# Optimization experiments

Hardware: AMD Instinct MI355X
Metric: run time of the kernel (lower is better)

## Reference

```python
import jax, jax.numpy as jnp
import numpy as np

N_EXPERTS = 8
IN_DIM = 2048
HID_DIM = 4096  # max(IN_DIM*2, IN_DIM)
OUT_DIM = 2048
N_NODES = 16384


def setup_inputs() -> dict:
    key = jax.random.key(0)
    k1, k2, k3 = jax.random.split(key, 3)
    x = jax.random.normal(k1, (N_NODES, IN_DIM), dtype=jnp.float32)
    # nn.init.normal_(std=0.02); torch Linear stores weight as [out, in]
    W1 = jax.random.normal(k2, (N_EXPERTS, HID_DIM, IN_DIM), dtype=jnp.float32) * 0.02
    W2 = jax.random.normal(k3, (N_EXPERTS, OUT_DIM, HID_DIM), dtype=jnp.float32) * 0.02
    return {"expert_idx": 2, "x": x, "W1": W1, "W2": W2}


def reference(expert_idx, x, W1, W2):
    # Select this expert's weights (static index, matches ModuleList lookup)
    w1 = W1[expert_idx]  # [hid, in]
    w2 = W2[expert_idx]  # [out, hid]
    h = jnp.einsum('ni,hi->nh', x, w1)          # Linear(in->hid), bias=False
    h = jax.nn.gelu(h, approximate=False)        # torch nn.GELU default = exact erf
    out = jnp.einsum('nh,oh->no', h, w2)         # Linear(hid->out), bias=False
    return out
```

## Files before the change

### kernel.cpp

```cpp
#include <hip/hip_runtime.h>
#include <hip/hip_bf16.h>
#include <math.h>


typedef __bf16 bf16x8 __attribute__((ext_vector_type(8)));
typedef float floatx4 __attribute__((ext_vector_type(4)));

#define GLD16(gp, lp)                                                          \
  __builtin_amdgcn_global_load_lds(                                            \
      (__attribute__((address_space(1))) void*)(gp),                           \
      (__attribute__((address_space(3))) void*)(lp), 16, 0, 0)

__device__ __forceinline__ unsigned short f2bf(float f) {
  union { float f; unsigned int u; } v; v.f = f;
  unsigned int r = v.u + 0x7fffu + ((v.u >> 16) & 1u);
  return (unsigned short)(r >> 16);
}

__global__ void sniff_kernel(const unsigned short* __restrict__ x,
                             int* __restrict__ flag) {
  int lane = threadIdx.x & 63;
  unsigned short u = x[lane * 2];
  int e = (u >> 7) & 0xFF;
  bool ok = (e >= 118) && (e <= 133);
  unsigned long long m = __ballot(ok ? 1 : 0);
  if (lane == 0) flag[0] = (__popcll(m) > 32) ? 1 : 0;
}

__global__ void cvt_kernel(const float* __restrict__ in,
                           unsigned short* __restrict__ out,
                           const int* __restrict__ idxp, long long expert_stride,
                           const int* __restrict__ flagp) {
  if (flagp[0]) return;
  long long base = idxp ? (long long)idxp[0] * expert_stride : 0;
  long long i = ((long long)blockIdx.x * blockDim.x + threadIdx.x) * 4;
  float4 v = *(const float4*)(in + base + i);
  ushort4 o;
  o.x = f2bf(v.x); o.y = f2bf(v.y); o.z = f2bf(v.z); o.w = f2bf(v.w);
  *(ushort4*)(out + i) = o;
}

template <bool GELU, int N, int K>
__global__ __launch_bounds__(512, 2) void gemm256(
    const unsigned short* __restrict__ Aws,
    const unsigned short* __restrict__ Araw,
    const unsigned short* __restrict__ Bws,
    const unsigned short* __restrict__ Braw,
    const int* __restrict__ idxp, long long expert_stride,
    void* __restrict__ Cv, const int* __restrict__ flagp) {
  const int flag = flagp[0];
  const unsigned short* __restrict__ A = flag ? Araw : Aws;
  const unsigned short* __restrict__ B =
      flag ? (Braw + (long long)idxp[0] * expert_stride) : Bws;

  extern __shared__ __align__(16) char smem[];

  constexpr int NT = K / 32;
  constexpr int NTN = N / 256;

  const int nwg = (int)gridDim.x;
  const int cpx = nwg >> 3;
  const int bid = (int)blockIdx.x;
  const int swz = (bid & 7) * cpx + (bid >> 3);
  const int m0 = (swz / NTN) * 256;
  const int n0 = (swz % NTN) * 256;

  const int tid  = (int)threadIdx.x;
  const int lane = tid & 63;
  const int wave = tid >> 6;
  const int lrow = lane & 15;
  const int quad = lane >> 4;
  const int wm = (wave >> 2) * 128;
  const int wn = (wave & 3) * 64;

  auto decode = [](int u, int& r, int& c) {
    int s = u >> 3, cw = u & 7;
    int cp = cw ^ (s & 7);
    r = (s << 1) | (cp >> 2);
    c = cp & 3;
  };
  int ra0, ca0, ra1, ca1;
  decode(tid, ra0, ca0);
  decode(tid + 512, ra1, ca1);
  const unsigned short* gA0 = A + (long long)(m0 + ra0) * K + ca0 * 8;
  const unsigned short* gA1 = A + (long long)(m0 + ra1) * K + ca1 * 8;
  const unsigned short* gB0 = B + (long long)(n0 + ra0) * K + ca0 * 8;
  const unsigned short* gB1 = B + (long long)(n0 + ra1) * K + ca1 * 8;

  auto STAGE = [&](int t) {
    char* bb = smem + (t & 3) * 32768;
    GLD16(gA0 + t * 32, bb + tid * 16);
    GLD16(gA1 + t * 32, bb + 8192 + tid * 16);
    GLD16(gB0 + t * 32, bb + 16384 + tid * 16);
    GLD16(gB1 + t * 32, bb + 24576 + tid * 16);
  };

  const int cpp = (quad | ((lrow & 1) << 2)) ^ ((lrow >> 1) & 7);
  const int aoff = wm * 64 + (lrow >> 1) * 128 + cpp * 16;
  const int boff = wn * 64 + (lrow >> 1) * 128 + cpp * 16;

  floatx4 acc[8][4] = {};

  STAGE(0); STAGE(1); STAGE(2);
  asm volatile("s_waitcnt vmcnt(8)" ::: "memory");
  __builtin_amdgcn_s_barrier();
  asm volatile("" ::: "memory");

#pragma unroll 4
  for (int t = 0; t < NT; ++t) {
    char* bb = smem + (t & 3) * 32768;
    const char* Ab = bb + aoff;
    const char* Bb = bb + 16384 + boff;
    bf16x8 a[8], b[4];
#pragma unroll
    for (int j = 0; j < 4; ++j) b[j] = *(const bf16x8*)(Bb + j * 1024);
#pragma unroll
    for (int i = 0; i < 4; ++i) a[i] = *(const bf16x8*)(Ab + i * 1024);
    if (t + 3 < NT) STAGE(t + 3);
#pragma unroll
    for (int i = 4; i < 8; ++i) a[i] = *(const bf16x8*)(Ab + i * 1024);
    __builtin_amdgcn_s_setprio(1);
#pragma unroll
    for (int i = 0; i < 8; ++i)
#pragma unroll
      for (int j = 0; j < 4; ++j)
        acc[i][j] = __builtin_amdgcn_mfma_f32_16x16x32_bf16(a[i], b[j],
                                                            acc[i][j], 0, 0, 0);
    __builtin_amdgcn_s_setprio(0);
    if (t + 1 < NT) {
      if (t + 3 < NT)      asm volatile("s_waitcnt vmcnt(8)" ::: "memory");
      else if (t + 2 < NT) asm volatile("s_waitcnt vmcnt(4)" ::: "memory");
      else                 asm volatile("s_waitcnt vmcnt(0)" ::: "memory");
      __builtin_amdgcn_s_barrier();
      asm volatile("" ::: "memory");
    }
  }

  if (GELU) {
    unsigned short* Cp = (unsigned short*)Cv;
#pragma unroll
    for (int i = 0; i < 8; ++i) {
      const int rb = m0 + wm + i * 16 + quad * 4;
#pragma unroll
      for (int j = 0; j < 4; ++j) {
        const int col = n0 + wn + j * 16 + lrow;
#pragma unroll
        for (int r = 0; r < 4; ++r) {
          float v = acc[i][j][r];
          v = 0.5f * v * (1.0f + erff(v * 0.70710678118654752f));
          Cp[(long long)(rb + r) * N + col] = f2bf(v);
        }
      }
    }
  } else if (flag) {
    unsigned short* Cp = (unsigned short*)Cv;
#pragma unroll
    for (int i = 0; i < 8; ++i) {
      const int rb = m0 + wm + i * 16 + quad * 4;
#pragma unroll
      for (int j = 0; j < 4; ++j) {
        const int col = n0 + wn + j * 16 + lrow;
#pragma unroll
        for (int r = 0; r < 4; ++r)
          Cp[(long long)(rb + r) * N + col] = f2bf(acc[i][j][r]);
      }
    }
  } else {
    float* Cp = (float*)Cv;
#pragma unroll
    for (int i = 0; i < 8; ++i) {
      const int rb = m0 + wm + i * 16 + quad * 4;
#pragma unroll
      for (int j = 0; j < 4; ++j) {
        const int col = n0 + wn + j * 16 + lrow;
#pragma unroll
        for (int r = 0; r < 4; ++r)
          Cp[(long long)(rb + r) * N + col] = acc[i][j][r];
      }
    }
  }
}

extern "C" void kernel_launch(void* const* d_in, const int* in_sizes, int n_in,
                              void* d_out, int out_size, void* d_ws,
                              size_t ws_size, hipStream_t stream) {
  const int* idxp = (const int*)d_in[0];
  const void* x  = d_in[1];
  const void* W1 = d_in[2];
  const void* W2 = d_in[3];

  char* ws = (char*)d_ws;
  int* flag = (int*)ws;
  unsigned short* h   = (unsigned short*)(ws + 256);
  unsigned short* xb  = (unsigned short*)(ws + 256 + 134217728LL);
  unsigned short* w1b = xb + 33554432LL;
  unsigned short* w2b = w1b + 8388608LL;

  (void)hipFuncSetAttribute((const void*)gemm256<true, 4096, 2048>,
                            hipFuncAttributeMaxDynamicSharedMemorySize, 131072);
  (void)hipFuncSetAttribute((const void*)gemm256<false, 2048, 4096>,
                            hipFuncAttributeMaxDynamicSharedMemorySize, 131072);

  sniff_kernel<<<dim3(1), dim3(64), 0, stream>>>((const unsigned short*)x, flag);

  cvt_kernel<<<dim3(32768), dim3(256), 0, stream>>>((const float*)x, xb,
                                                    nullptr, 0, flag);
  cvt_kernel<<<dim3(8192), dim3(256), 0, stream>>>((const float*)W1, w1b,
                                                   idxp, 8388608LL, flag);
  cvt_kernel<<<dim3(8192), dim3(256), 0, stream>>>((const float*)W2, w2b,
                                                   idxp, 8388608LL, flag);

  gemm256<true, 4096, 2048><<<dim3(1024), dim3(512), 131072, stream>>>(
      xb, (const unsigned short*)x, w1b, (const unsigned short*)W1, idxp,
      8388608LL, h, flag);

  gemm256<false, 2048, 4096><<<dim3(512), dim3(512), 131072, stream>>>(
      h, h, w2b, (const unsigned short*)W2, idxp, 8388608LL, d_out, flag);
}
```

Before: 1.098 ms.

## Restructure GEMM main loop into double-buffered 64-K ping-pong with split A/B staging

Replaces the 4-deep ring of 32-K LDS stages with two 64-K buffers, each split into two K-halves. A and B tiles are staged separately. Each iteration runs four MFMA phases, and each phase is separated by a barrier and an interleaved global-to-LDS prefetch. This follows the HipKittens-style 8-wave ping-pong pattern, meant to overlap loads with MFMA more finely and to lower register pressure by holding only 4 A fragments at once. It adds more barriers per K step, and the vmcnt accounting in the tail iterations is fragile.

```diff
diff --git a/kernel.cpp b/kernel.cpp
--- a/kernel.cpp
+++ b/kernel.cpp
@@ -10,6 +10,11 @@
   __builtin_amdgcn_global_load_lds(                                            \
       (__attribute__((address_space(1))) void*)(gp),                           \
       (__attribute__((address_space(3))) void*)(lp), 16, 0, 0)
+
+#define WAITV8() asm volatile("s_waitcnt vmcnt(8)" ::: "memory")
+#define WAITV4() asm volatile("s_waitcnt vmcnt(4)" ::: "memory")
+#define WAITV0() asm volatile("s_waitcnt vmcnt(0)" ::: "memory")
+#define BAR()    asm volatile("s_barrier" ::: "memory")
 
 __device__ __forceinline__ unsigned short f2bf(float f) {
   union { float f; unsigned int u; } v; v.f = f;
@@ -55,7 +60,7 @@
 
   extern __shared__ __align__(16) char smem[];
 
-  constexpr int NT = K / 32;
+  constexpr int NT2 = K / 64;
   constexpr int NTN = N / 256;
 
   const int nwg = (int)gridDim.x;
@@ -82,17 +87,20 @@
   int ra0, ca0, ra1, ca1;
   decode(tid, ra0, ca0);
   decode(tid + 512, ra1, ca1);
-  const unsigned short* gA0 = A + (long long)(m0 + ra0) * K + ca0 * 8;
-  const unsigned short* gA1 = A + (long long)(m0 + ra1) * K + ca1 * 8;
-  const unsigned short* gB0 = B + (long long)(n0 + ra0) * K + ca0 * 8;
-  const unsigned short* gB1 = B + (long long)(n0 + ra1) * K + ca1 * 8;
-
-  auto STAGE = [&](int t) {
-    char* bb = smem + (t & 3) * 32768;
-    GLD16(gA0 + t * 32, bb + tid * 16);
-    GLD16(gA1 + t * 32, bb + 8192 + tid * 16);
-    GLD16(gB0 + t * 32, bb + 16384 + tid * 16);
-    GLD16(gB1 + t * 32, bb + 24576 + tid * 16);
+  const unsigned short* pA0 = A + (long long)(m0 + ra0) * K + ca0 * 8;
+  const unsigned short* pA1 = A + (long long)(m0 + ra1) * K + ca1 * 8;
+  const unsigned short* pB0 = B + (long long)(n0 + ra0) * K + ca0 * 8;
+  const unsigned short* pB1 = B + (long long)(n0 + ra1) * K + ca1 * 8;
+
+  auto STAGE_A = [&](int t, int kk) {
+    char* base = smem + (t & 1) * 65536 + kk * 16384;
+    GLD16(pA0 + t * 64 + kk * 32, base + tid * 16);
+    GLD16(pA1 + t * 64 + kk * 32, base + 8192 + tid * 16);
+  };
+  auto STAGE_B = [&](int t, int kk) {
+    char* base = smem + (t & 1) * 65536 + 32768 + kk * 16384;
+    GLD16(pB0 + t * 64 + kk * 32, base + tid * 16);
+    GLD16(pB1 + t * 64 + kk * 32, base + 8192 + tid * 16);
   };
 
   const int cpp = (quad | ((lrow & 1) << 2)) ^ ((lrow >> 1) & 7);
@@ -101,39 +109,78 @@
 
   floatx4 acc[8][4] = {};
 
-  STAGE(0); STAGE(1); STAGE(2);
-  asm volatile("s_waitcnt vmcnt(8)" ::: "memory");
-  __builtin_amdgcn_s_barrier();
-  asm volatile("" ::: "memory");
-
-#pragma unroll 4
-  for (int t = 0; t < NT; ++t) {
-    char* bb = smem + (t & 3) * 32768;
-    const char* Ab = bb + aoff;
-    const char* Bb = bb + 16384 + boff;
-    bf16x8 a[8], b[4];
-#pragma unroll
-    for (int j = 0; j < 4; ++j) b[j] = *(const bf16x8*)(Bb + j * 1024);
-#pragma unroll
-    for (int i = 0; i < 4; ++i) a[i] = *(const bf16x8*)(Ab + i * 1024);
-    if (t + 3 < NT) STAGE(t + 3);
-#pragma unroll
-    for (int i = 4; i < 8; ++i) a[i] = *(const bf16x8*)(Ab + i * 1024);
-    __builtin_amdgcn_s_setprio(1);
-#pragma unroll
-    for (int i = 0; i < 8; ++i)
-#pragma unroll
-      for (int j = 0; j < 4; ++j)
-        acc[i][j] = __builtin_amdgcn_mfma_f32_16x16x32_bf16(a[i], b[j],
-                                                            acc[i][j], 0, 0, 0);
-    __builtin_amdgcn_s_setprio(0);
-    if (t + 1 < NT) {
-      if (t + 3 < NT)      asm volatile("s_waitcnt vmcnt(8)" ::: "memory");
-      else if (t + 2 < NT) asm volatile("s_waitcnt vmcnt(4)" ::: "memory");
-      else                 asm volatile("s_waitcnt vmcnt(0)" ::: "memory");
-      __builtin_amdgcn_s_barrier();
-      asm volatile("" ::: "memory");
-    }
+  STAGE_A(0, 0); STAGE_B(0, 0); STAGE_A(0, 1); STAGE_B(0, 1);
+  STAGE_A(1, 0); STAGE_B(1, 0);
+  WAITV8();
+  BAR();
+
+#pragma unroll 2
+  for (int T = 0; T < NT2; ++T) {
+    const char* Ak0 = smem + (T & 1) * 65536 + aoff;
+    const char* Bk0 = smem + (T & 1) * 65536 + 32768 + boff;
+    bf16x8 a[4], b0[4], b1[4];
+
+#pragma unroll
+    for (int n = 0; n < 4; ++n) b0[n] = *(const bf16x8*)(Bk0 + n * 1024);
+#pragma unroll
+    for (int m = 0; m < 4; ++m) a[m] = *(const bf16x8*)(Ak0 + m * 1024);
+    if (T + 1 < NT2) STAGE_A(T + 1, 1);
+    BAR();
+    __builtin_amdgcn_s_setprio(1);
+#pragma unroll
+    for (int m = 0; m < 4; ++m)
+#pragma unroll
+      for (int n = 0; n < 4; ++n)
+        acc[m][n] = __builtin_amdgcn_mfma_f32_16x16x32_bf16(a[m], b0[n],
+                                                            acc[m][n], 0, 0, 0);
+    __builtin_amdgcn_s_setprio(0);
+
+#pragma unroll
+    for (int m = 0; m < 4; ++m)
+      a[m] = *(const bf16x8*)(Ak0 + (4 + m) * 1024);
+    if (T + 1 < NT2) STAGE_B(T + 1, 1);
+    if (T < NT2 - 1) { WAITV8(); } else { WAITV0(); }
+    BAR();
+    __builtin_amdgcn_s_setprio(1);
+#pragma unroll
+    for (int m = 0; m < 4; ++m)
+#pragma unroll
+      for (int n = 0; n < 4; ++n)
+        acc[4 + m][n] = __builtin_amdgcn_mfma_f32_16x16x32_bf16(
+            a[m], b0[n], acc[4 + m][n], 0, 0, 0);
+    __builtin_amdgcn_s_setprio(0);
+
+#pragma unroll
+    for (int n = 0; n < 4; ++n)
+      b1[n] = *(const bf16x8*)(Bk0 + 16384 + n * 1024);
+#pragma unroll
+    for (int m = 0; m < 4; ++m)
+      a[m] = *(const bf16x8*)(Ak0 + 16384 + m * 1024);
+    if (T + 2 < NT2) STAGE_A(T + 2, 0);
+    BAR();
+    __builtin_amdgcn_s_setprio(1);
+#pragma unroll
+    for (int m = 0; m < 4; ++m)
+#pragma unroll
+      for (int n = 0; n < 4; ++n)
+        acc[m][n] = __builtin_amdgcn_mfma_f32_16x16x32_bf16(a[m], b1[n],
+                                                            acc[m][n], 0, 0, 0);
+    __builtin_amdgcn_s_setprio(0);
+
+#pragma unroll
+    for (int m = 0; m < 4; ++m)
+      a[m] = *(const bf16x8*)(Ak0 + 16384 + (4 + m) * 1024);
+    if (T + 2 < NT2) STAGE_B(T + 2, 0);
+    if (T < NT2 - 2) { WAITV8(); } else if (T == NT2 - 2) { WAITV4(); }
+    BAR();
+    __builtin_amdgcn_s_setprio(1);
+#pragma unroll
+    for (int m = 0; m < 4; ++m)
+#pragma unroll
+      for (int n = 0; n < 4; ++n)
+        acc[4 + m][n] = __builtin_amdgcn_mfma_f32_16x16x32_bf16(
+            a[m], b1[n], acc[4 + m][n], 0, 0, 0);
+    __builtin_amdgcn_s_setprio(0);
   }
 
   if (GELU) {
```

Result: faster. 1.050 ms (-4.4%).
